# Kernel tuning notes

Hardware: AMD Instinct MI355X
Metric: run time of the kernel (lower is better)

The kernel has to match this reference:

```python
import jax, jax.numpy as jnp
import numpy as np

P = 113          # vocab (modulus)
D = 128          # residual_dim
H = 4            # n_heads (hardcoded in Model)
DH = D // H      # head_dim = 32
HID = 4 * D      # mlp hidden = 512
BATCH = 131072
RATE = 0.5       # attention_rate


def setup_inputs() -> dict:
    key = jax.random.key(0)
    ks = jax.random.split(key, 12)
    std = 1.0 / D ** 0.5
    x = jax.random.randint(ks[0], (BATCH, 2), 0, P)
    tok_emb = jax.random.normal(ks[1], (P, D), jnp.float32) / D ** 0.5
    pos_emb = jax.random.normal(ks[2], (2, D), jnp.float32) / D ** 0.5
    W_Q = jax.random.normal(ks[3], (H, D, DH), jnp.float32) * std
    W_K = jax.random.normal(ks[4], (H, D, DH), jnp.float32) * std
    W_V = jax.random.normal(ks[5], (H, D, DH), jnp.float32) * std
    W_O = jax.random.normal(ks[6], (H, DH, D), jnp.float32) * std
    # nn.Linear default init: U(-1/sqrt(fan_in), 1/sqrt(fan_in))
    b1_bound = 1.0 / D ** 0.5
    W1 = jax.random.uniform(ks[7], (D, HID), jnp.float32, -b1_bound, b1_bound)
    b1 = jax.random.uniform(ks[8], (HID,), jnp.float32, -b1_bound, b1_bound)
    b2_bound = 1.0 / HID ** 0.5
    W2 = jax.random.uniform(ks[9], (HID, D), jnp.float32, -b2_bound, b2_bound)
    b2 = jax.random.uniform(ks[10], (D,), jnp.float32, -b2_bound, b2_bound)
    W_U = jax.random.normal(ks[11], (P, D), jnp.float32) / P ** 0.5
    return dict(x=x, tok_emb=tok_emb, pos_emb=pos_emb, W_Q=W_Q, W_K=W_K,
                W_V=W_V, W_O=W_O, W1=W1, b1=b1, W2=W2, b2=b2, W_U=W_U)


def reference(x, tok_emb, pos_emb, W_Q, W_K, W_V, W_O, W1, b1, W2, b2, W_U):
    # embed: [B,2,D]
    resid = tok_emb[x] + pos_emb[None, :, :]
    # attention
    q = jnp.einsum('bpd,hdk->bphk', resid, W_Q)
    k = jnp.einsum('bpd,hdk->bphk', resid, W_K)
    v = jnp.einsum('bpd,hdk->bphk', resid, W_V)
    scores = jnp.einsum('bqhk,bshk->bhqs', q, k) / DH ** 0.5  # [B,H,2,2]
    pattern = jax.nn.softmax(scores, axis=-1)
    pattern = (1.0 - RATE) + RATE * pattern  # uniform blend, no causal mask
    z = jnp.einsum('bshk,bhqs->bqhk', v, pattern)
    attn_out = jnp.einsum('bqhk,hkd->bqd', z, W_O)
    resid = resid + attn_out
    # mlp
    h = jax.nn.relu(resid @ W1 + b1)
    resid = resid + (h @ W2 + b2)
    # unembed: [B,2,P]
    logits = jnp.einsum('vd,bpd->bpv', W_U, resid)
    return logits
```

## Files before the change

### kernel.cpp

```cpp
#include <hip/hip_runtime.h>
#include <hip/hip_bf16.h>
#include <stdint.h>

typedef __hip_bfloat16 bf16;
typedef __attribute__((ext_vector_type(8))) short short8;
typedef __attribute__((ext_vector_type(4))) float float4v;
typedef __attribute__((ext_vector_type(2))) float f2v;

#define NVOCAB 113
#define NPAIR (113 * 113)
#define DDIM 128
#define HIDDIM 512
#define PAIRS_PB 16
#define ROWS_PB 32

#define OFF_B1  145792
#define OFF_B2  211840

#define BOFF_WOT 0
#define BOFF_W1T 16384
#define BOFF_W2T (16384 + 65536)
#define BOFF_WUP (16384 + 65536 + 65536)
#define BTOTAL   (16384 + 65536 + 65536 + 16384)

__device__ __forceinline__ uint16_t f2b(float f) {
  bf16 h = __float2bfloat16(f);
  return *(uint16_t*)&h;
}
__device__ __forceinline__ float b2f(uint16_t u) {
  return __uint_as_float(((uint32_t)u) << 16);
}
__device__ __forceinline__ float ldsrc(const void* p, int i, int isb) {
  return isb ? b2f(((const uint16_t*)p)[i]) : ((const float*)p)[i];
}

__device__ __forceinline__ void bar_lds() {
  asm volatile("s_waitcnt lgkmcnt(0)\n\ts_barrier" ::: "memory");
}

__device__ __forceinline__ int detect_isb(const uint32_t* __restrict__ tok_raw) {
  uint32_t u = tok_raw[threadIdx.x & 63];
  int e = (u >> 7) & 0xff;
  unsigned long long m = __ballot(e >= 100 && e <= 126);
  return __popcll(m) >= 48;
}

struct SrcPtrs { const void* p[11]; };

__global__ void __launch_bounds__(384) build_kernel(
    SrcPtrs sp, float* __restrict__ wf,
    float* __restrict__ resid_pre, float* __restrict__ qt,
    float* __restrict__ kt, float* __restrict__ vt,
    uint16_t* __restrict__ wb) {
  const int tid = threadIdx.x;
  const int blk = blockIdx.x;
  const int isb = detect_isb((const uint32_t*)sp.p[0]);

  if (blk < 226) {
    const int row = blk;
    const int t = row >> 1, p = row & 1;
    __shared__ float r[DDIM];
    if (tid < DDIM) {
      float rv = ldsrc(sp.p[0], t * DDIM + tid, isb) +
                 ldsrc(sp.p[1], p * DDIM + tid, isb);
      r[tid] = rv;
      resid_pre[row * DDIM + tid] = rv;
    }
    __syncthreads();
    const int which = tid >> 7, jj = tid & 127;
    const int h = jj >> 5, j = jj & 31;
    const void* wsrc = sp.p[2 + which];
    const int base = h * 4096 + j;
    float a = 0.f;
    if (isb) {
      const uint16_t* w16 = (const uint16_t*)wsrc;
      #pragma unroll 8
      for (int d = 0; d < 128; ++d)
        a += r[d] * b2f(w16[base + d * 32]);
    } else {
      const float* w32 = (const float*)wsrc;
      #pragma unroll 8
      for (int d = 0; d < 128; ++d)
        a += r[d] * w32[base + d * 32];
    }
    float* outp = (which == 0) ? qt : (which == 1) ? kt : vt;
    outp[row * DDIM + jj] = a;
  } else if (blk < 653) {
    const int idx = (blk - 226) * 384 + tid;
    if (idx < BTOTAL) {
      float v;
      if (idx < BOFF_W1T) {
        int l = idx, d = l >> 7, c = l & 127;
        v = ldsrc(sp.p[5], c * 128 + d, isb);
      } else if (idx < BOFF_W2T) {
        int l = idx - BOFF_W1T, n = l >> 7, d = l & 127;
        v = ldsrc(sp.p[6], d * 512 + n, isb);
      } else if (idx < BOFF_WUP) {
        int l = idx - BOFF_W2T, d = l >> 9, j = l & 511;
        v = ldsrc(sp.p[8], j * 128 + d, isb);
      } else {
        int l = idx - BOFF_WUP, vv = l >> 7, d = l & 127;
        v = (vv < NVOCAB) ? ldsrc(sp.p[10], vv * 128 + d, isb) : 0.f;
      }
      wb[idx] = f2b(v);
    }
  } else {
    const int i = (blk - 653) * 384 + tid;
    if (i < 512) wf[OFF_B1 + i] = ldsrc(sp.p[7], i, isb);
    else if (i < 640) wf[OFF_B2 + (i - 512)] = ldsrc(sp.p[9], i - 512, isb);
  }
}

__global__ void __launch_bounds__(512, 2) pair_mfma_kernel(
    const float* __restrict__ resid_pre, const float* __restrict__ qt,
    const float* __restrict__ kt, const float* __restrict__ vt,
    const float* __restrict__ wf, const uint16_t* __restrict__ wb,
    float* __restrict__ table) {
  __shared__ uint16_t bufH[ROWS_PB * 512];
  __shared__ uint16_t bufZ[ROWS_PB * 128];
  __shared__ uint16_t bufS[ROWS_PB * 128];
  __shared__ float    spat[PAIRS_PB * 16];

  const int tid = threadIdx.x;
  const int blk = blockIdx.x;
  const int lane = tid & 63;
  const int npar = tid >> 6;
  const int l15 = lane & 15, quad = lane >> 4;

  #define ROW_OF(row_) ({                                        \
    int pr_ = blk * PAIRS_PB + ((row_) >> 1);                    \
    if (pr_ >= NPAIR) pr_ = NPAIR - 1;                           \
    int t0_ = pr_ / NVOCAB, t1_ = pr_ - t0_ * NVOCAB;            \
    ((row_) & 1) ? t1_ * 2 + 1 : t0_ * 2; })

  const int nG = npar * 16 + l15;

  short8 bW0[4];
  {
    const uint16_t* bp = wb + BOFF_WOT + nG * 128 + quad * 8;
    #pragma unroll
    for (int ks = 0; ks < 4; ++ks) bW0[ks] = *(const short8*)(bp + ks * 32);
  }

  float rpre[2][4];
  #pragma unroll
  for (int mf = 0; mf < 2; ++mf)
    #pragma unroll
    for (int r = 0; r < 4; ++r)
      rpre[mf][r] = resid_pre[ROW_OF(mf * 16 + quad * 4 + r) * DDIM + nG];
  float bias1v[4];
  #pragma unroll
  for (int ni = 0; ni < 4; ++ni)
    bias1v[ni] = wf[OFF_B1 + (npar + ni * 8) * 16 + l15];
  const float bias2 = wf[OFF_B2 + nG];
  const int zm = tid >> 4, zc0 = (tid & 15) * 8;
  float4 zv0a, zv0b, zv1a, zv1b;
  {
    const int zr0 = ROW_OF((zm >> 1) * 2);
    const int zr1 = ROW_OF((zm >> 1) * 2 + 1);
    const float4* p0 = (const float4*)(vt + zr0 * DDIM + zc0);
    const float4* p1 = (const float4*)(vt + zr1 * DDIM + zc0);
    zv0a = p0[0]; zv0b = p0[1]; zv1a = p1[0]; zv1b = p1[1];
  }

  if (tid < 128) {
    const int pl = tid >> 3, s = tid & 7;
    int pair = blk * PAIRS_PB + pl;
    if (pair >= NPAIR) pair = NPAIR - 1;
    const int t0 = pair / NVOCAB, t1 = pair - t0 * NVOCAB;
    const int row0 = t0 * 2, row1 = t1 * 2 + 1;
    const int h = s >> 1, qp = s & 1;
    const float4* qrow = (const float4*)(qt + (qp ? row1 : row0) * DDIM + h * 32);
    const float4* k0r  = (const float4*)(kt + row0 * DDIM + h * 32);
    const float4* k1r  = (const float4*)(kt + row1 * DDIM + h * 32);
    float acc0 = 0.f, acc1 = 0.f;
    #pragma unroll
    for (int j = 0; j < 8; ++j) {
      float4 qv = qrow[j], kv0 = k0r[j], kv1 = k1r[j];
      acc0 += qv.x * kv0.x + qv.y * kv0.y + qv.z * kv0.z + qv.w * kv0.w;
      acc1 += qv.x * kv1.x + qv.y * kv1.y + qv.z * kv1.z + qv.w * kv1.w;
    }
    float s0 = acc0 * 0.17677669529663687f;
    float s1 = acc1 * 0.17677669529663687f;
    float m = fmaxf(s0, s1);
    float e0 = __expf(s0 - m), e1 = __expf(s1 - m);
    float inv = 1.f / (e0 + e1);
    spat[pl * 16 + s * 2]     = 0.5f + 0.5f * e0 * inv;
    spat[pl * 16 + s * 2 + 1] = 0.5f + 0.5f * e1 * inv;
  }
  bar_lds();

  {
    const int pl = zm >> 1, qp = zm & 1;
    const int h = zc0 >> 5;
    const float p0 = spat[pl * 16 + h * 4 + qp * 2];
    const float p1 = spat[pl * 16 + h * 4 + qp * 2 + 1];
    float v0[8] = {zv0a.x, zv0a.y, zv0a.z, zv0a.w, zv0b.x, zv0b.y, zv0b.z, zv0b.w};
    float v1[8] = {zv1a.x, zv1a.y, zv1a.z, zv1a.w, zv1b.x, zv1b.y, zv1b.z, zv1b.w};
    short8 pk;
    #pragma unroll
    for (int e = 0; e < 8; ++e)
      pk[e] = (short)f2b(p0 * v0[e] + p1 * v1[e]);
    *(short8*)&bufZ[(zm * 16 + ((zc0 >> 3) ^ (zm & 15))) * 8] = pk;
  }
  bar_lds();

  float smid[2][4];
  short8 bW1a[2][4];

  {
    short8 af[2][4];
    #pragma unroll
    for (int mf = 0; mf < 2; ++mf)
      #pragma unroll
      for (int ks = 0; ks < 4; ++ks)
        af[mf][ks] = *(const short8*)&bufZ[((mf * 16 + l15) * 16 +
                                           ((ks * 4 + quad) ^ l15)) * 8];
    float4v acc[2] = {{0.f, 0.f, 0.f, 0.f}, {0.f, 0.f, 0.f, 0.f}};
    #pragma unroll
    for (int mf = 0; mf < 2; ++mf)
      #pragma unroll
      for (int ks = 0; ks < 4; ++ks)
        acc[mf] = __builtin_amdgcn_mfma_f32_16x16x32_bf16(af[mf][ks], bW0[ks],
                                                          acc[mf], 0, 0, 0);
    #pragma unroll
    for (int nj = 0; nj < 2; ++nj) {
      const int n = (npar + nj * 8) * 16 + l15;
      const uint16_t* bp = wb + BOFF_W1T + n * 128 + quad * 8;
      #pragma unroll
      for (int ks = 0; ks < 4; ++ks)
        bW1a[nj][ks] = *(const short8*)(bp + ks * 32);
    }
    #pragma unroll
    for (int mf = 0; mf < 2; ++mf)
      #pragma unroll
      for (int r = 0; r < 4; ++r) {
        const int row = mf * 16 + quad * 4 + r;
        float v = acc[mf][r] + rpre[mf][r];
        smid[mf][r] = v;
        bufS[(row * 16 + ((nG >> 3) ^ (row & 15))) * 8 + (nG & 7)] = f2b(v);
      }
  }
  bar_lds();

  short8 bB2a[8];

  {
    short8 af[2][4];
    #pragma unroll
    for (int mf = 0; mf < 2; ++mf)
      #pragma unroll
      for (int ks = 0; ks < 4; ++ks)
        af[mf][ks] = *(const short8*)&bufS[((mf * 16 + l15) * 16 +
                                           ((ks * 4 + quad) ^ l15)) * 8];
    #pragma unroll
    for (int nj = 0; nj < 2; ++nj) {
      const int ni = nj;
      const int n = (npar + ni * 8) * 16 + l15;
      float4v acc[2] = {{0.f, 0.f, 0.f, 0.f}, {0.f, 0.f, 0.f, 0.f}};
      #pragma unroll
      for (int mf = 0; mf < 2; ++mf)
        #pragma unroll
        for (int ks = 0; ks < 4; ++ks)
          acc[mf] = __builtin_amdgcn_mfma_f32_16x16x32_bf16(
              af[mf][ks], bW1a[nj][ks], acc[mf], 0, 0, 0);
      const float bias = bias1v[ni];
      #pragma unroll
      for (int mf = 0; mf < 2; ++mf)
        #pragma unroll
        for (int r = 0; r < 4; ++r) {
          const int row = mf * 16 + quad * 4 + r;
          bufH[(row * 64 + ((n >> 3) ^ (row & 15))) * 8 + (n & 7)] =
              f2b(fmaxf(acc[mf][r] + bias, 0.f));
        }
    }
    short8 bW1b[2][4];
    #pragma unroll
    for (int nj = 0; nj < 2; ++nj) {
      const int n = (npar + (2 + nj) * 8) * 16 + l15;
      const uint16_t* bp = wb + BOFF_W1T + n * 128 + quad * 8;
      #pragma unroll
      for (int ks = 0; ks < 4; ++ks)
        bW1b[nj][ks] = *(const short8*)(bp + ks * 32);
    }
    #pragma unroll
    for (int nj = 0; nj < 2; ++nj) {
      const int ni = 2 + nj;
      const int n = (npar + ni * 8) * 16 + l15;
      float4v acc[2] = {{0.f, 0.f, 0.f, 0.f}, {0.f, 0.f, 0.f, 0.f}};
      #pragma unroll
      for (int mf = 0; mf < 2; ++mf)
        #pragma unroll
        for (int ks = 0; ks < 4; ++ks)
          acc[mf] = __builtin_amdgcn_mfma_f32_16x16x32_bf16(
              af[mf][ks], bW1b[nj][ks], acc[mf], 0, 0, 0);
      const float bias = bias1v[ni];
      #pragma unroll
      for (int mf = 0; mf < 2; ++mf)
        #pragma unroll
        for (int r = 0; r < 4; ++r) {
          const int row = mf * 16 + quad * 4 + r;
          bufH[(row * 64 + ((n >> 3) ^ (row & 15))) * 8 + (n & 7)] =
              f2b(fmaxf(acc[mf][r] + bias, 0.f));
        }
    }
    {
      const uint16_t* bp = wb + BOFF_W2T + nG * 512 + quad * 8;
      #pragma unroll
      for (int k8 = 0; k8 < 8; ++k8)
        bB2a[k8] = *(const short8*)(bp + k8 * 32);
    }
  }
  bar_lds();

  short8 bW3[4];

  {
    const uint16_t* bp = wb + BOFF_W2T + nG * 512 + quad * 8;
    float4v acc0 = {0.f, 0.f, 0.f, 0.f};
    float4v acc1 = {0.f, 0.f, 0.f, 0.f};
    #pragma unroll
    for (int qtr = 0; qtr < 2; ++qtr) {
      short8 a0[4], a1[4];
      #pragma unroll
      for (int k4 = 0; k4 < 4; ++k4) {
        const int ks = qtr * 4 + k4;
        a0[k4] = *(const short8*)&bufH[(l15 * 64 + ((ks * 4 + quad) ^ l15)) * 8];
        a1[k4] = *(const short8*)&bufH[((16 + l15) * 64 +
                                       ((ks * 4 + quad) ^ l15)) * 8];
      }
      #pragma unroll
      for (int k4 = 0; k4 < 4; ++k4) {
        acc0 = __builtin_amdgcn_mfma_f32_16x16x32_bf16(
            a0[k4], bB2a[qtr * 4 + k4], acc0, 0, 0, 0);
        acc1 = __builtin_amdgcn_mfma_f32_16x16x32_bf16(
            a1[k4], bB2a[qtr * 4 + k4], acc1, 0, 0, 0);
      }
    }
    short8 bB2b[8];
    #pragma unroll
    for (int k8 = 0; k8 < 8; ++k8)
      bB2b[k8] = *(const short8*)(bp + (8 + k8) * 32);
    #pragma unroll
    for (int qtr = 0; qtr < 2; ++qtr) {
      short8 a0[4], a1[4];
      #pragma unroll
      for (int k4 = 0; k4 < 4; ++k4) {
        const int ks = 8 + qtr * 4 + k4;
        a0[k4] = *(const short8*)&bufH[(l15 * 64 + ((ks * 4 + quad) ^ l15)) * 8];
        a1[k4] = *(const short8*)&bufH[((16 + l15) * 64 +
                                       ((ks * 4 + quad) ^ l15)) * 8];
      }
      #pragma unroll
      for (int k4 = 0; k4 < 4; ++k4) {
        acc0 = __builtin_amdgcn_mfma_f32_16x16x32_bf16(
            a0[k4], bB2b[qtr * 4 + k4], acc0, 0, 0, 0);
        acc1 = __builtin_amdgcn_mfma_f32_16x16x32_bf16(
            a1[k4], bB2b[qtr * 4 + k4], acc1, 0, 0, 0);
      }
    }
    {
      const uint16_t* bp3 = wb + BOFF_WUP + nG * 128 + quad * 8;
      #pragma unroll
      for (int ks = 0; ks < 4; ++ks)
        bW3[ks] = *(const short8*)(bp3 + ks * 32);
    }
    #pragma unroll
    for (int r = 0; r < 4; ++r) {
      const int row0 = quad * 4 + r;
      const int row1 = 16 + quad * 4 + r;
      bufZ[(row0 * 16 + ((nG >> 3) ^ (row0 & 15))) * 8 + (nG & 7)] =
          f2b(acc0[r] + bias2 + smid[0][r]);
      bufZ[(row1 * 16 + ((nG >> 3) ^ (row1 & 15))) * 8 + (nG & 7)] =
          f2b(acc1[r] + bias2 + smid[1][r]);
    }
  }
  bar_lds();

  {
    short8 ar[2][4];
    #pragma unroll
    for (int mf = 0; mf < 2; ++mf)
      #pragma unroll
      for (int ks = 0; ks < 4; ++ks)
        ar[mf][ks] = *(const short8*)&bufZ[((mf * 16 + l15) * 16 +
                                           ((ks * 4 + quad) ^ l15)) * 8];
    float4v acc[2] = {{0.f, 0.f, 0.f, 0.f}, {0.f, 0.f, 0.f, 0.f}};
    #pragma unroll
    for (int mf = 0; mf < 2; ++mf)
      #pragma unroll
      for (int ks = 0; ks < 4; ++ks)
        acc[mf] = __builtin_amdgcn_mfma_f32_16x16x32_bf16(ar[mf][ks], bW3[ks],
                                                          acc[mf], 0, 0, 0);
    if (nG < NVOCAB) {
      #pragma unroll
      for (int mf = 0; mf < 2; ++mf)
        #pragma unroll
        for (int r = 0; r < 4; ++r) {
          const int row = mf * 16 + quad * 4 + r;
          const int pair = blk * PAIRS_PB + (row >> 1);
          if (pair < NPAIR)
            table[pair * 226 + (row & 1) * 113 + nG] = acc[mf][r];
        }
    }
  }
  #undef ROW_OF
}

__global__ void gather_kernel(const uint32_t* __restrict__ x_raw,
                              const f2v* __restrict__ table2,
                              f2v* __restrict__ out2, int total) {
  uint32_t xs = x_raw[2 * (threadIdx.x & 63) + 1];
  unsigned long long nz = __ballot(xs != 0u);
  const int is64 = (nz == 0ull);

  const int i = blockIdx.x * 256 + threadIdx.x;
  if (i >= total) return;
  const int b = i / NVOCAB;
  const int j = i - b * NVOCAB;
  int t0, t1;
  if (is64) {
    t0 = (int)x_raw[4 * b];
    t1 = (int)x_raw[4 * b + 2];
  } else {
    t0 = (int)x_raw[2 * b];
    t1 = (int)x_raw[2 * b + 1];
  }
  t0 = min(max(t0, 0), NVOCAB - 1);
  t1 = min(max(t1, 0), NVOCAB - 1);
  const int pair = t0 * NVOCAB + t1;
  f2v v = table2[(size_t)pair * NVOCAB + j];
  __builtin_nontemporal_store(v, &out2[i]);
}

extern "C" void kernel_launch(void* const* d_in, const int* in_sizes, int n_in,
                              void* d_out, int out_size, void* d_ws, size_t ws_size,
                              hipStream_t stream) {
  float*    wf        = (float*)((char*)d_ws + 256);
  float*    resid_pre = (float*)((char*)d_ws + 905984);
  float*    qt        = (float*)((char*)d_ws + 1021696);
  float*    kt        = (float*)((char*)d_ws + 1137408);
  float*    vt        = (float*)((char*)d_ws + 1253120);
  float*    table     = (float*)((char*)d_ws + 1368832);
  uint16_t* wb        = (uint16_t*)((char*)d_ws + 12912016);

  const int B = in_sizes[0] / 2;

  SrcPtrs sp;
  for (int i = 0; i < 11; ++i) sp.p[i] = d_in[i + 1];

  build_kernel<<<655, 384, 0, stream>>>(sp, wf, resid_pre, qt, kt, vt, wb);

  const int nblk = (NPAIR + PAIRS_PB - 1) / PAIRS_PB;
  pair_mfma_kernel<<<nblk, 512, 0, stream>>>(resid_pre, qt, kt, vt, wf, wb,
                                             table);

  const int total = B * NVOCAB;
  gather_kernel<<<(total + 255) / 256, 256, 0, stream>>>(
      (const uint32_t*)d_in[0], (const f2v*)table, (f2v*)d_out, total);
}
```

Before: 243.9 us.

## Prefetch weight fragments a full stage ahead with inline-asm loads and waits

Weight B-fragments for W1, W2 and W_U are now loaded with inline-asm global_load_dwordx4 one stage before they are used. Explicit s_waitcnt vmcnt(0) barriers tied to the destination registers control when the data must arrive. This stops the compiler from placing waits right after each load, so global memory latency can overlap the previous stage's MFMA and LDS work. The cost is much higher register pressure (all 16 W1 and 16 W2 fragments are live at once), which may lower occupancy or cause spills. The vmcnt(0) waits also block on every outstanding load, including unrelated ones.

```diff
diff --git a/kernel.cpp b/kernel.cpp
--- a/kernel.cpp
+++ b/kernel.cpp
@@ -37,6 +37,17 @@
 __device__ __forceinline__ void bar_lds() {
   asm volatile("s_waitcnt lgkmcnt(0)\n\ts_barrier" ::: "memory");
 }
+
+__device__ __forceinline__ short8 gl16(const uint16_t* p) {
+  short8 r;
+  asm volatile("global_load_dwordx4 %0, %1, off" : "=v"(r) : "v"(p));
+  return r;
+}
+#define VMW4(a0,a1,a2,a3) \
+  asm volatile("s_waitcnt vmcnt(0)" : "+v"(a0),"+v"(a1),"+v"(a2),"+v"(a3))
+#define VMW8(a0,a1,a2,a3,a4,a5,a6,a7) \
+  asm volatile("s_waitcnt vmcnt(0)" : "+v"(a0),"+v"(a1),"+v"(a2),"+v"(a3), \
+                                      "+v"(a4),"+v"(a5),"+v"(a6),"+v"(a7))
 
 __device__ __forceinline__ int detect_isb(const uint32_t* __restrict__ tok_raw) {
   uint32_t u = tok_raw[threadIdx.x & 63];
@@ -138,8 +149,8 @@
   short8 bW0[4];
   {
     const uint16_t* bp = wb + BOFF_WOT + nG * 128 + quad * 8;
-    #pragma unroll
-    for (int ks = 0; ks < 4; ++ks) bW0[ks] = *(const short8*)(bp + ks * 32);
+    bW0[0] = gl16(bp);       bW0[1] = gl16(bp + 32);
+    bW0[2] = gl16(bp + 64);  bW0[3] = gl16(bp + 96);
   }
 
   float rpre[2][4];
@@ -206,7 +217,7 @@
   bar_lds();
 
   float smid[2][4];
-  short8 bW1a[2][4];
+  short8 bW1[4][4];
 
   {
     short8 af[2][4];
@@ -216,6 +227,15 @@
       for (int ks = 0; ks < 4; ++ks)
         af[mf][ks] = *(const short8*)&bufZ[((mf * 16 + l15) * 16 +
                                            ((ks * 4 + quad) ^ l15)) * 8];
+    VMW4(bW0[0], bW0[1], bW0[2], bW0[3]);
+    #pragma unroll
+    for (int ni = 0; ni < 4; ++ni) {
+      const int n = (npar + ni * 8) * 16 + l15;
+      const uint16_t* bp = wb + BOFF_W1T + n * 128 + quad * 8;
+      #pragma unroll
+      for (int ks = 0; ks < 4; ++ks)
+        bW1[ni][ks] = gl16(bp + ks * 32);
+    }
     float4v acc[2] = {{0.f, 0.f, 0.f, 0.f}, {0.f, 0.f, 0.f, 0.f}};
     #pragma unroll
     for (int mf = 0; mf < 2; ++mf)
@@ -223,14 +243,6 @@
       for (int ks = 0; ks < 4; ++ks)
         acc[mf] = __builtin_amdgcn_mfma_f32_16x16x32_bf16(af[mf][ks], bW0[ks],
                                                           acc[mf], 0, 0, 0);
-    #pragma unroll
-    for (int nj = 0; nj < 2; ++nj) {
-      const int n = (npar + nj * 8) * 16 + l15;
-      const uint16_t* bp = wb + BOFF_W1T + n * 128 + quad * 8;
-      #pragma unroll
-      for (int ks = 0; ks < 4; ++ks)
-        bW1a[nj][ks] = *(const short8*)(bp + ks * 32);
-    }
     #pragma unroll
     for (int mf = 0; mf < 2; ++mf)
       #pragma unroll
@@ -243,7 +255,7 @@
   }
   bar_lds();
 
-  short8 bB2a[8];
+  short8 bB2[16];
 
   {
     short8 af[2][4];
@@ -253,9 +265,18 @@
       for (int ks = 0; ks < 4; ++ks)
         af[mf][ks] = *(const short8*)&bufS[((mf * 16 + l15) * 16 +
                                            ((ks * 4 + quad) ^ l15)) * 8];
-    #pragma unroll
-    for (int nj = 0; nj < 2; ++nj) {
-      const int ni = nj;
+    VMW8(bW1[0][0], bW1[0][1], bW1[0][2], bW1[0][3],
+         bW1[1][0], bW1[1][1], bW1[1][2], bW1[1][3]);
+    VMW8(bW1[2][0], bW1[2][1], bW1[2][2], bW1[2][3],
+         bW1[3][0], bW1[3][1], bW1[3][2], bW1[3][3]);
+    {
+      const uint16_t* bp = wb + BOFF_W2T + nG * 512 + quad * 8;
+      #pragma unroll
+      for (int k8 = 0; k8 < 16; ++k8)
+        bB2[k8] = gl16(bp + k8 * 32);
+    }
+    #pragma unroll
+    for (int ni = 0; ni < 4; ++ni) {
       const int n = (npar + ni * 8) * 16 + l15;
       float4v acc[2] = {{0.f, 0.f, 0.f, 0.f}, {0.f, 0.f, 0.f, 0.f}};
       #pragma unroll
@@ -263,7 +284,7 @@
         #pragma unroll
         for (int ks = 0; ks < 4; ++ks)
           acc[mf] = __builtin_amdgcn_mfma_f32_16x16x32_bf16(
-              af[mf][ks], bW1a[nj][ks], acc[mf], 0, 0, 0);
+              af[mf][ks], bW1[ni][ks], acc[mf], 0, 0, 0);
       const float bias = bias1v[ni];
       #pragma unroll
       for (int mf = 0; mf < 2; ++mf)
@@ -274,96 +295,43 @@
               f2b(fmaxf(acc[mf][r] + bias, 0.f));
         }
     }
-    short8 bW1b[2][4];
-    #pragma unroll
-    for (int nj = 0; nj < 2; ++nj) {
-      const int n = (npar + (2 + nj) * 8) * 16 + l15;
-      const uint16_t* bp = wb + BOFF_W1T + n * 128 + quad * 8;
-      #pragma unroll
-      for (int ks = 0; ks < 4; ++ks)
-        bW1b[nj][ks] = *(const short8*)(bp + ks * 32);
-    }
-    #pragma unroll
-    for (int nj = 0; nj < 2; ++nj) {
-      const int ni = 2 + nj;
-      const int n = (npar + ni * 8) * 16 + l15;
-      float4v acc[2] = {{0.f, 0.f, 0.f, 0.f}, {0.f, 0.f, 0.f, 0.f}};
-      #pragma unroll
-      for (int mf = 0; mf < 2; ++mf)
-        #pragma unroll
-        for (int ks = 0; ks < 4; ++ks)
-          acc[mf] = __builtin_amdgcn_mfma_f32_16x16x32_bf16(
-              af[mf][ks], bW1b[nj][ks], acc[mf], 0, 0, 0);
-      const float bias = bias1v[ni];
-      #pragma unroll
-      for (int mf = 0; mf < 2; ++mf)
-        #pragma unroll
-        for (int r = 0; r < 4; ++r) {
-          const int row = mf * 16 + quad * 4 + r;
-          bufH[(row * 64 + ((n >> 3) ^ (row & 15))) * 8 + (n & 7)] =
-              f2b(fmaxf(acc[mf][r] + bias, 0.f));
-        }
-    }
+  }
+  bar_lds();
+
+  short8 bW3[4];
+
+  {
+    VMW8(bB2[0], bB2[1], bB2[2],  bB2[3],  bB2[4],  bB2[5],  bB2[6],  bB2[7]);
+    VMW8(bB2[8], bB2[9], bB2[10], bB2[11], bB2[12], bB2[13], bB2[14], bB2[15]);
     {
-      const uint16_t* bp = wb + BOFF_W2T + nG * 512 + quad * 8;
-      #pragma unroll
-      for (int k8 = 0; k8 < 8; ++k8)
-        bB2a[k8] = *(const short8*)(bp + k8 * 32);
-    }
-  }
-  bar_lds();
-
-  short8 bW3[4];
-
-  {
-    const uint16_t* bp = wb + BOFF_W2T + nG * 512 + quad * 8;
+      const uint16_t* bp3 = wb + BOFF_WUP + nG * 128 + quad * 8;
+      bW3[0] = gl16(bp3);       bW3[1] = gl16(bp3 + 32);
+      bW3[2] = gl16(bp3 + 64);  bW3[3] = gl16(bp3 + 96);
+    }
     float4v acc0 = {0.f, 0.f, 0.f, 0.f};
     float4v acc1 = {0.f, 0.f, 0.f, 0.f};
     #pragma unroll
-    for (int qtr = 0; qtr < 2; ++qtr) {
-      short8 a0[4], a1[4];
-      #pragma unroll
-      for (int k4 = 0; k4 < 4; ++k4) {
-        const int ks = qtr * 4 + k4;
-        a0[k4] = *(const short8*)&bufH[(l15 * 64 + ((ks * 4 + quad) ^ l15)) * 8];
-        a1[k4] = *(const short8*)&bufH[((16 + l15) * 64 +
-                                       ((ks * 4 + quad) ^ l15)) * 8];
+    for (int half = 0; half < 2; ++half) {
+      #pragma unroll
+      for (int qtr = 0; qtr < 2; ++qtr) {
+        short8 a0[4], a1[4];
+        #pragma unroll
+        for (int k4 = 0; k4 < 4; ++k4) {
+          const int ks = half * 8 + qtr * 4 + k4;
+          a0[k4] = *(const short8*)&bufH[(l15 * 64 +
+                                         ((ks * 4 + quad) ^ l15)) * 8];
+          a1[k4] = *(const short8*)&bufH[((16 + l15) * 64 +
+                                         ((ks * 4 + quad) ^ l15)) * 8];
+        }
+        #pragma unroll
+        for (int k4 = 0; k4 < 4; ++k4) {
+          const int ks = half * 8 + qtr * 4 + k4;
+          acc0 = __builtin_amdgcn_mfma_f32_16x16x32_bf16(
+              a0[k4], bB2[ks], acc0, 0, 0, 0);
+          acc1 = __builtin_amdgcn_mfma_f32_16x16x32_bf16(
+              a1[k4], bB2[ks], acc1, 0, 0, 0);
+        }
       }
-      #pragma unroll
-      for (int k4 = 0; k4 < 4; ++k4) {
-        acc0 = __builtin_amdgcn_mfma_f32_16x16x32_bf16(
-            a0[k4], bB2a[qtr * 4 + k4], acc0, 0, 0, 0);
-        acc1 = __builtin_amdgcn_mfma_f32_16x16x32_bf16(
-            a1[k4], bB2a[qtr * 4 + k4], acc1, 0, 0, 0);
-      }
-    }
-    short8 bB2b[8];
-    #pragma unroll
-    for (int k8 = 0; k8 < 8; ++k8)
-      bB2b[k8] = *(const short8*)(bp + (8 + k8) * 32);
-    #pragma unroll
-    for (int qtr = 0; qtr < 2; ++qtr) {
-      short8 a0[4], a1[4];
-      #pragma unroll
-      for (int k4 = 0; k4 < 4; ++k4) {
-        const int ks = 8 + qtr * 4 + k4;
-        a0[k4] = *(const short8*)&bufH[(l15 * 64 + ((ks * 4 + quad) ^ l15)) * 8];
-        a1[k4] = *(const short8*)&bufH[((16 + l15) * 64 +
-                                       ((ks * 4 + quad) ^ l15)) * 8];
-      }
-      #pragma unroll
-      for (int k4 = 0; k4 < 4; ++k4) {
-        acc0 = __builtin_amdgcn_mfma_f32_16x16x32_bf16(
-            a0[k4], bB2b[qtr * 4 + k4], acc0, 0, 0, 0);
-        acc1 = __builtin_amdgcn_mfma_f32_16x16x32_bf16(
-            a1[k4], bB2b[qtr * 4 + k4], acc1, 0, 0, 0);
-      }
-    }
-    {
-      const uint16_t* bp3 = wb + BOFF_WUP + nG * 128 + quad * 8;
-      #pragma unroll
-      for (int ks = 0; ks < 4; ++ks)
-        bW3[ks] = *(const short8*)(bp3 + ks * 32);
     }
     #pragma unroll
     for (int r = 0; r < 4; ++r) {
@@ -385,6 +353,7 @@
       for (int ks = 0; ks < 4; ++ks)
         ar[mf][ks] = *(const short8*)&bufZ[((mf * 16 + l15) * 16 +
                                            ((ks * 4 + quad) ^ l15)) * 8];
+    VMW4(bW3[0], bW3[1], bW3[2], bW3[3]);
     float4v acc[2] = {{0.f, 0.f, 0.f, 0.f}, {0.f, 0.f, 0.f, 0.f}};
     #pragma unroll
     for (int mf = 0; mf < 2; ++mf)
```

Result: no change. 243.8 us (-0.1%).
